# Optimization experiments

Measured on AMD Instinct MI355X. Metric: run time of the kernel, lower is better.

The kernel has to match this reference:

```python
import jax, jax.numpy as jnp
import numpy as np

WINDOW_SIZE = 11
SIGMA = 1.5
C1 = 0.01 ** 2
C2 = 0.03 ** 2


def _make_window(channel, dtype=jnp.float32):
    # Faithful to torch `gaussian`: center at window_size/2 (= 5.5 for ws=11)
    x = np.arange(WINDOW_SIZE, dtype=np.float64)
    g = np.exp(-((x - WINDOW_SIZE / 2) ** 2) / (2.0 * SIGMA ** 2))
    g = (g / g.sum()).astype(np.float32)
    w2d = np.outer(g, g)  # (ws, ws)
    w = np.broadcast_to(w2d, (channel, 1, WINDOW_SIZE, WINDOW_SIZE)).copy()
    return jnp.asarray(w, dtype=dtype)


def _dwconv(x, w, channel):
    pad = WINDOW_SIZE // 2
    return jax.lax.conv_general_dilated(
        x, w,
        window_strides=(1, 1),
        padding=[(pad, pad), (pad, pad)],
        dimension_numbers=("NCHW", "OIHW", "NCHW"),
        feature_group_count=channel,
    )


def setup_inputs() -> dict:
    key = jax.random.key(0)
    k1, k2 = jax.random.split(key)
    B, C, H, W = 16, 3, 512, 512
    img1 = jax.random.uniform(k1, (B, C, H, W), dtype=jnp.float32)
    img2 = jax.random.uniform(k2, (B, C, H, W), dtype=jnp.float32)
    return {"img1": img1, "img2": img2}


def reference(img1, img2):
    channel = img1.shape[1]
    window = _make_window(channel, img1.dtype)

    mu1 = _dwconv(img1, window, channel)
    mu2 = _dwconv(img2, window, channel)
    mu1_sq = mu1 * mu1
    mu2_sq = mu2 * mu2
    mu1_mu2 = mu1 * mu2

    sigma1_sq = _dwconv(img1 * img1, window, channel) - mu1_sq
    sigma2_sq = _dwconv(img2 * img2, window, channel) - mu2_sq
    sigma12 = _dwconv(img1 * img2, window, channel) - mu1_mu2

    numerator = (2 * mu1_mu2 + C1) * (2 * sigma12 + C2)
    denominator = (mu1_sq + mu2_sq + C1) * (sigma1_sq + sigma2_sq + C2)
    ssim_map = numerator / denominator
    return jnp.mean(ssim_map)  # size_average=True
```

## Files before the change

kernel.cpp:

```cpp
#include <hip/hip_runtime.h>
#include <cmath>


#define IMG_H 512
#define IMG_W 512
#define STRIPE 32
#define NSTR (IMG_H / STRIPE)
#define NPLANES 48
#define NBLOCKS (NPLANES * NSTR)
#define SSIM_C1 (0.01f * 0.01f)
#define SSIM_C2 (0.03f * 0.03f)

typedef float f32x2 __attribute__((ext_vector_type(2)));

struct W2x11 { float2 w[11]; };

__launch_bounds__(512, 2)
__global__ void ssim_main(const float* __restrict__ img1,
                          const float* __restrict__ img2,
                          float* __restrict__ blockSums, W2x11 wv) {
    __shared__ float2 tb[2][528];
    __shared__ float red[8];

    const int x = threadIdx.x;
    const int bid = blockIdx.x;
    const int plane = bid >> 4;
    const int stripe = bid & (NSTR - 1);
    const int y0 = stripe * STRIPE;
    const size_t base = (size_t)plane * (IMG_H * IMG_W);

    if (x < 10) {
        const int col = (x < 5) ? x : (x + 512);
        tb[0][col] = make_float2(0.f, 0.f);
        tb[1][col] = make_float2(0.f, 0.f);
    }

    f32x2 rAB[11], rSP[11];
    float acc = 0.f;

    float pa = 0.f, pb = 0.f;
    {
        const int r0 = y0 - 5;
        if (r0 >= 0) {
            pa = img1[base + (size_t)r0 * IMG_W + x];
            pb = img2[base + (size_t)r0 * IMG_W + x];
        }
    }

    int buf = 0;
#pragma unroll 1
    for (int c = 0; c < 4; ++c) {
#pragma unroll
        for (int j = 0; j < 11; ++j) {
            const int i = c * 11 + j;
            if (i < 42) {
                tb[buf][x + 5] = make_float2(pa, pb);
                pa = 0.f; pb = 0.f;
                const int rn = y0 - 4 + i;
                if (i + 1 < 42 && rn >= 0 && rn < IMG_H) {
                    pa = img1[base + (size_t)rn * IMG_W + x];
                    pb = img2[base + (size_t)rn * IMG_W + x];
                }
                __syncthreads();
                f32x2 hAB = {0.f, 0.f}, hSP = {0.f, 0.f};
#pragma unroll
                for (int k = 0; k < 11; ++k) {
                    const float2 t = tb[buf][x + k];
                    f32x2 ab; ab.x = t.x; ab.y = t.y;
                    f32x2 sp;
                    sp.x = fmaf(t.y, t.y, t.x * t.x);
                    sp.y = t.x * t.y;
                    f32x2 w2; w2.x = wv.w[k].x; w2.y = wv.w[k].y;
                    hAB = __builtin_elementwise_fma(w2, ab, hAB);
                    hSP = __builtin_elementwise_fma(w2, sp, hSP);
                }
                rAB[j] = hAB; rSP[j] = hSP;

                if (i >= 10) {
                    f32x2 vAB = {0.f, 0.f}, vSP = {0.f, 0.f};
#pragma unroll
                    for (int k = 0; k < 11; ++k) {
                        const int s = (j + 1 + k) % 11;
                        f32x2 w2; w2.x = wv.w[k].x; w2.y = wv.w[k].y;
                        vAB = __builtin_elementwise_fma(w2, rAB[s], vAB);
                        vSP = __builtin_elementwise_fma(w2, rSP[s], vSP);
                    }
                    const float vA = vAB.x, vB = vAB.y;
                    const float vS = vSP.x, vP = vSP.y;
                    const float mu11 = vA * vA;
                    const float mu22 = vB * vB;
                    const float mu12 = vA * vB;
                    const float num = fmaf(2.f, mu12, SSIM_C1) *
                                      fmaf(2.f, vP - mu12, SSIM_C2);
                    const float d1  = mu11 + mu22;
                    const float den = (d1 + SSIM_C1) * ((vS - d1) + SSIM_C2);
                    acc = fmaf(num, __builtin_amdgcn_rcpf(den), acc);
                }
                buf ^= 1;
            }
        }
    }

#pragma unroll
    for (int off = 32; off >= 1; off >>= 1)
        acc += __shfl_down(acc, off, 64);
    const int wave = x >> 6, lane = x & 63;
    if (lane == 0) red[wave] = acc;
    __syncthreads();
    if (x == 0) {
        float s = 0.f;
#pragma unroll
        for (int k = 0; k < 8; ++k) s += red[k];
        blockSums[bid] = s;
    }
}

__global__ void ssim_reduce(const float* __restrict__ bs,
                            float* __restrict__ out) {
    __shared__ double red[4];
    const int t = threadIdx.x;
    double a = 0.0;
    for (int idx = t; idx < NBLOCKS; idx += 256) a += (double)bs[idx];
#pragma unroll
    for (int off = 32; off >= 1; off >>= 1)
        a += __shfl_down(a, off, 64);
    const int wave = t >> 6, lane = t & 63;
    if (lane == 0) red[wave] = a;
    __syncthreads();
    if (t == 0) {
        const double s = red[0] + red[1] + red[2] + red[3];
        out[0] = (float)(s / (double)((double)NPLANES * IMG_H * IMG_W));
    }
}

extern "C" void kernel_launch(void* const* d_in, const int* in_sizes, int n_in,
                              void* d_out, int out_size, void* d_ws, size_t ws_size,
                              hipStream_t stream) {
    const float* img1 = (const float*)d_in[0];
    const float* img2 = (const float*)d_in[1];
    float* out = (float*)d_out;
    float* bs = (float*)d_ws;

    W2x11 wv;
    double g[11], s = 0.0;
    for (int i = 0; i < 11; ++i) {
        const double d = (double)i - 5.5;
        g[i] = exp(-(d * d) / (2.0 * 1.5 * 1.5));
        s += g[i];
    }
    for (int i = 0; i < 11; ++i) {
        const float w = (float)(g[i] / s);
        wv.w[i] = make_float2(w, w);
    }

    ssim_main<<<NBLOCKS, 512, 0, stream>>>(img1, img2, bs, wv);
    ssim_reduce<<<1, 256, 0, stream>>>(bs, out);
}
```

Before: 149.5 us.

## Use sum/difference basis for SSIM moments and deepen row-load prefetch

Each loaded pixel pair is stored as (a+b, a-b), so the horizontal pass squares one packed vector instead of computing a*a+b*b and a*b separately. The SSIM terms are then recovered algebraically from the filtered sums, differences and squared quantities. The row loop is unrolled over 22 rows with two rows of loads kept in flight, which hides more global-memory latency. The cost is more live registers and slightly different floating-point rounding from the change of basis.

```diff
diff --git a/kernel.cpp b/kernel.cpp
--- a/kernel.cpp
+++ b/kernel.cpp
@@ -18,7 +18,7 @@
 __launch_bounds__(512, 2)
 __global__ void ssim_main(const float* __restrict__ img1,
                           const float* __restrict__ img2,
-                          float* __restrict__ blockSums, W2x11 wv) {
+                          float* __restrict__ blockSums, W2x11 wvp) {
     __shared__ float2 tb[2][528];
     __shared__ float red[8];
 
@@ -35,65 +35,75 @@
         tb[1][col] = make_float2(0.f, 0.f);
     }
 
-    f32x2 rAB[11], rSP[11];
+    f32x2 rSD[11], rQ[11];
     float acc = 0.f;
 
-    float pa = 0.f, pb = 0.f;
+    float pea = 0.f, peb = 0.f, poa = 0.f, pob = 0.f;
     {
         const int r0 = y0 - 5;
+        const int r1 = y0 - 4;
         if (r0 >= 0) {
-            pa = img1[base + (size_t)r0 * IMG_W + x];
-            pb = img2[base + (size_t)r0 * IMG_W + x];
+            pea = img1[base + (size_t)r0 * IMG_W + x];
+            peb = img2[base + (size_t)r0 * IMG_W + x];
+        }
+        if (r1 >= 0) {
+            poa = img1[base + (size_t)r1 * IMG_W + x];
+            pob = img2[base + (size_t)r1 * IMG_W + x];
         }
     }
 
     int buf = 0;
 #pragma unroll 1
-    for (int c = 0; c < 4; ++c) {
+    for (int c = 0; c < 2; ++c) {
 #pragma unroll
-        for (int j = 0; j < 11; ++j) {
-            const int i = c * 11 + j;
+        for (int j = 0; j < 22; ++j) {
+            const int i = c * 22 + j;
             if (i < 42) {
-                tb[buf][x + 5] = make_float2(pa, pb);
-                pa = 0.f; pb = 0.f;
-                const int rn = y0 - 4 + i;
-                if (i + 1 < 42 && rn >= 0 && rn < IMG_H) {
-                    pa = img1[base + (size_t)rn * IMG_W + x];
-                    pb = img2[base + (size_t)rn * IMG_W + x];
+                const float pa = (j & 1) ? poa : pea;
+                const float pb = (j & 1) ? pob : peb;
+                tb[buf][x + 5] = make_float2(pa + pb, pa - pb);
+                {
+                    float na = 0.f, nb = 0.f;
+                    const int rn = y0 - 3 + i;
+                    if (i + 2 < 42 && rn >= 0 && rn < IMG_H) {
+                        const size_t rb = base + (size_t)rn * IMG_W;
+                        na = img1[rb + x];
+                        nb = img2[rb + x];
+                    }
+                    if (j & 1) { poa = na; pob = nb; }
+                    else       { pea = na; peb = nb; }
                 }
                 __syncthreads();
-                f32x2 hAB = {0.f, 0.f}, hSP = {0.f, 0.f};
+                f32x2 hSD = {0.f, 0.f}, hQ = {0.f, 0.f};
 #pragma unroll
                 for (int k = 0; k < 11; ++k) {
                     const float2 t = tb[buf][x + k];
-                    f32x2 ab; ab.x = t.x; ab.y = t.y;
-                    f32x2 sp;
-                    sp.x = fmaf(t.y, t.y, t.x * t.x);
-                    sp.y = t.x * t.y;
-                    f32x2 w2; w2.x = wv.w[k].x; w2.y = wv.w[k].y;
-                    hAB = __builtin_elementwise_fma(w2, ab, hAB);
-                    hSP = __builtin_elementwise_fma(w2, sp, hSP);
+                    f32x2 sd; sd.x = t.x; sd.y = t.y;
+                    const f32x2 q = sd * sd;
+                    f32x2 w2; w2.x = wvp.w[k].x; w2.y = wvp.w[k].y;
+                    hSD = __builtin_elementwise_fma(w2, sd, hSD);
+                    hQ  = __builtin_elementwise_fma(w2, q,  hQ);
                 }
-                rAB[j] = hAB; rSP[j] = hSP;
+                rSD[j % 11] = hSD;
+                rQ [j % 11] = hQ;
 
                 if (i >= 10) {
-                    f32x2 vAB = {0.f, 0.f}, vSP = {0.f, 0.f};
+                    f32x2 vSD = {0.f, 0.f}, vQ = {0.f, 0.f};
 #pragma unroll
                     for (int k = 0; k < 11; ++k) {
                         const int s = (j + 1 + k) % 11;
-                        f32x2 w2; w2.x = wv.w[k].x; w2.y = wv.w[k].y;
-                        vAB = __builtin_elementwise_fma(w2, rAB[s], vAB);
-                        vSP = __builtin_elementwise_fma(w2, rSP[s], vSP);
+                        f32x2 w2; w2.x = wvp.w[k].x; w2.y = wvp.w[k].y;
+                        vSD = __builtin_elementwise_fma(w2, rSD[s], vSD);
+                        vQ  = __builtin_elementwise_fma(w2, rQ[s],  vQ);
                     }
-                    const float vA = vAB.x, vB = vAB.y;
-                    const float vS = vSP.x, vP = vSP.y;
-                    const float mu11 = vA * vA;
-                    const float mu22 = vB * vB;
-                    const float mu12 = vA * vB;
-                    const float num = fmaf(2.f, mu12, SSIM_C1) *
-                                      fmaf(2.f, vP - mu12, SSIM_C2);
-                    const float d1  = mu11 + mu22;
-                    const float den = (d1 + SSIM_C1) * ((vS - d1) + SSIM_C2);
+                    const float ss = vSD.x * vSD.x;
+                    const float dd = vSD.y * vSD.y;
+                    const float e1 = (ss - dd) * 0.5f;
+                    const float e2 = (ss + dd) * 0.5f;
+                    const float f1 = (vQ.x - vQ.y) * 0.5f;
+                    const float f2 = (vQ.x + vQ.y) * 0.5f;
+                    const float num = (e1 + SSIM_C1) * ((f1 - e1) + SSIM_C2);
+                    const float den = (e2 + SSIM_C1) * ((f2 - e2) + SSIM_C2);
                     acc = fmaf(num, __builtin_amdgcn_rcpf(den), acc);
                 }
                 buf ^= 1;
```

Result: slower. 166.2 us (+11.2%).
